# Performance work log

Hardware: AMD Instinct MI355X
Metric: run time of the kernel (lower is better)

The kernel has to match this reference:

```python
import jax, jax.numpy as jnp
import numpy as np

NUM_NODES = 100000
FEAT_DIM = 256
H1 = 256
H2 = 256
NUM_CLASSES = 64
B = 4096
F1 = 25
F2 = 10


def setup_inputs() -> dict:
    key = jax.random.key(0)
    k0, k1, k2, ke, kw1, kw2, kw3 = jax.random.split(key, 7)
    T0 = jax.random.randint(k0, (B,), 0, NUM_NODES)
    T1 = jax.random.randint(k1, (B, F1), 0, NUM_NODES)
    T2 = jax.random.randint(k2, (B * F1, F2), 0, NUM_NODES)
    emb = jax.random.normal(ke, (NUM_NODES, FEAT_DIM), dtype=jnp.float32)
    # nn.Linear(in, out, bias=False) stores weight as [out, in]
    W1 = jax.random.normal(kw1, (H1, 2 * FEAT_DIM), dtype=jnp.float32) * (1.0 / np.sqrt(2 * FEAT_DIM))
    W2 = jax.random.normal(kw2, (H2, 2 * H1), dtype=jnp.float32) * (1.0 / np.sqrt(2 * H1))
    W3 = jax.random.normal(kw3, (NUM_CLASSES, H2), dtype=jnp.float32) * (1.0 / np.sqrt(H2))
    return {"T0": T0, "T1": T1, "T2": T2, "emb": emb, "W1": W1, "W2": W2, "W3": W3}


def reference(T0, T1, T2, emb, W1, W2, W3):
    # hop-0 roots: [B, D]; hop-1 neighbor mean: [B, D]
    feat_0 = emb[T0]
    x = emb[T1].mean(axis=1)
    h0 = jax.nn.relu(jnp.concatenate([feat_0, x], axis=1) @ W1.T)  # [B, H1]
    # dropout is identity in eval mode (p applied only in training)
    # hop-1 nodes with hop-2 neighbor mean: [B*F1, D] each
    feat_1 = emb[T1].reshape(-1, FEAT_DIM)
    x2 = emb[T2].mean(axis=1)  # [B*F1, D]
    h1 = jax.nn.relu(jnp.concatenate([feat_1, x2], axis=1) @ W1.T)  # [B*F1, H1]
    h1 = h1.reshape(B, F1, H1).mean(axis=1)  # [B, H1]
    combined = jnp.concatenate([h0, h1], axis=1)  # [B, 2*H1]
    embedding = jax.nn.relu(combined @ W2.T)  # [B, H2]
    scores = embedding @ W3.T  # [B, C]
    return scores
```

## Files before the change

kernel.cpp:

```cpp
#include <hip/hip_runtime.h>
#include <hip/hip_bf16.h>


typedef __bf16  bf16x8 __attribute__((ext_vector_type(8)));
typedef __bf16  bf16x4 __attribute__((ext_vector_type(4)));
typedef float   f32x4  __attribute__((ext_vector_type(4)));
typedef float   f32x2  __attribute__((ext_vector_type(2)));

#define BATCH     4096
#define F1        25
#define F2        10
#define NNODES    100000
#define ZY_NT     3125
#define ZY_BLOCKS 512

__device__ __forceinline__ uint2 pack4_bf16(float a, float b, float c, float d) {
    union { __bf16 h[4]; uint2 u; } p;
    p.h[0] = (__bf16)a; p.h[1] = (__bf16)b; p.h[2] = (__bf16)c; p.h[3] = (__bf16)d;
    return p.u;
}

__global__ __launch_bounds__(256) void cvt_bf16_8(const float* __restrict__ in,
                                                  __bf16* __restrict__ out, int n8) {
    int i = blockIdx.x * 256 + threadIdx.x;
    if (i < n8) {
        float4 v0 = reinterpret_cast<const float4*>(in)[i * 2];
        float4 v1 = reinterpret_cast<const float4*>(in)[i * 2 + 1];
        uint4 o;
        uint2 a = pack4_bf16(v0.x, v0.y, v0.z, v0.w);
        uint2 b = pack4_bf16(v1.x, v1.y, v1.z, v1.w);
        o.x = a.x; o.y = a.y; o.z = b.x; o.w = b.y;
        reinterpret_cast<uint4*>(out)[i] = o;
    }
}

__global__ __launch_bounds__(256) void prep_wzy(const float* __restrict__ W1,
                                                __bf16* __restrict__ Wzy) {
    int i = blockIdx.x * 256 + threadIdx.x;
    int r  = i >> 5;
    int c0 = (i & 31) * 8;
    const float* src = (r < 256) ? (W1 + (size_t)r * 512 + c0)
                                 : (W1 + (size_t)(r - 256) * 512 + 256 + c0);
    float4 a = reinterpret_cast<const float4*>(src)[0];
    float4 b = reinterpret_cast<const float4*>(src)[1];
    uint4 o;
    uint2 pa = pack4_bf16(a.x, a.y, a.z, a.w);
    uint2 pb = pack4_bf16(b.x, b.y, b.z, b.w);
    o.x = pa.x; o.y = pa.y; o.z = pb.x; o.w = pb.y;
    *reinterpret_cast<uint4*>(Wzy + (size_t)r * 256 + c0) = o;
}

__global__ __launch_bounds__(512, 2) void gemm_ZY(const float* __restrict__ emb,
                                                  const __bf16* __restrict__ Wzy,
                                                  __bf16* __restrict__ Ztab,
                                                  unsigned char* __restrict__ Y8) {
    __shared__ __align__(16) char Abuf[2][16384];
    __shared__ __align__(16) __bf16 Ybuf[8][32][72];
    const int tid  = threadIdx.x;
    const int wid  = tid >> 6;
    const int lane = tid & 63;
    const int lr   = lane & 15;
    const int kg   = lane >> 4;
    const int n0   = wid * 64;

    bf16x8 wfrag[4][8];
    {
        const __bf16* Wb = Wzy + (size_t)(n0 + lr) * 256 + kg * 8;
#pragma unroll
        for (int ni = 0; ni < 4; ++ni)
#pragma unroll
            for (int kt = 0; kt < 8; ++kt)
                wfrag[ni][kt] = *reinterpret_cast<const bf16x8*>(Wb + ni * 16 * 256 + kt * 32);
    }

    const int o0   = tid * 32;
    const int rs   = o0 >> 9;
    const int x0   = o0 & 511;
    const int sw0  = rs * 512 + ((x0)      ^ ((rs & 7) << 4));
    const int sw1  = rs * 512 + ((x0 + 16) ^ ((rs & 7) << 4));

    int t = blockIdx.x;
    float4 ld0[4];
    {
        const float4* src = reinterpret_cast<const float4*>(emb + (size_t)t * 8192 + tid * 16);
#pragma unroll
        for (int q = 0; q < 4; ++q) ld0[q] = src[q];
    }
    int cur = 0;

    for (; t < ZY_NT; t += ZY_BLOCKS) {
        {
            bf16x8 c0v, c1v;
#pragma unroll
            for (int e = 0; e < 4; ++e) {
                c0v[e]     = (__bf16)ld0[0][e];
                c0v[4 + e] = (__bf16)ld0[1][e];
                c1v[e]     = (__bf16)ld0[2][e];
                c1v[4 + e] = (__bf16)ld0[3][e];
            }
            *reinterpret_cast<bf16x8*>(Abuf[cur] + sw0) = c0v;
            *reinterpret_cast<bf16x8*>(Abuf[cur] + sw1) = c1v;
        }
        int tn = t + ZY_BLOCKS;
        float4 ld1[4] = {};
        if (tn < ZY_NT) {
            const float4* src = reinterpret_cast<const float4*>(emb + (size_t)tn * 8192 + tid * 16);
#pragma unroll
            for (int q = 0; q < 4; ++q) ld1[q] = src[q];
        }
        __syncthreads();

        f32x4 acc[2][4] = {};
        const char* Ab = Abuf[cur];
#pragma unroll
        for (int kt = 0; kt < 8; ++kt) {
            bf16x8 a[2];
#pragma unroll
            for (int mi = 0; mi < 2; ++mi) {
                int r  = mi * 16 + lr;
                int by = kt * 64 + kg * 16;
                a[mi] = *reinterpret_cast<const bf16x8*>(Ab + r * 512 + (by ^ ((r & 7) << 4)));
            }
#pragma unroll
            for (int mi = 0; mi < 2; ++mi)
#pragma unroll
                for (int ni = 0; ni < 4; ++ni)
                    acc[mi][ni] = __builtin_amdgcn_mfma_f32_16x16x32_bf16(a[mi], wfrag[ni][kt], acc[mi][ni], 0, 0, 0);
        }

        const int orow = (lane >> 4) * 4;
        const int ocol = lane & 15;
        const int m0   = t * 32;
#pragma unroll
        for (int mi = 0; mi < 2; ++mi)
#pragma unroll
            for (int ni = 0; ni < 4; ++ni)
#pragma unroll
                for (int j = 0; j < 4; ++j)
                    Ybuf[wid][mi * 16 + orow + j][ni * 16 + ocol] = (__bf16)acc[mi][ni][j];
        const int row = lane & 31;
        const int cg  = (lane >> 5) * 32;
        if (wid < 4) {
#pragma unroll
            for (int q = 0; q < 4; ++q) {
                bf16x8 v = *reinterpret_cast<bf16x8*>(&Ybuf[wid][row][cg + q * 8]);
                *reinterpret_cast<bf16x8*>(Ztab + (size_t)(m0 + row) * 256 + n0 + cg + q * 8) = v;
            }
        } else {
#pragma unroll
            for (int q = 0; q < 4; ++q) {
                bf16x8 v = *reinterpret_cast<bf16x8*>(&Ybuf[wid][row][cg + q * 8]);
                int w0 = 0, w1 = 0;
                w0 = __builtin_amdgcn_cvt_pk_fp8_f32((float)v[0], (float)v[1], w0, false);
                w0 = __builtin_amdgcn_cvt_pk_fp8_f32((float)v[2], (float)v[3], w0, true);
                w1 = __builtin_amdgcn_cvt_pk_fp8_f32((float)v[4], (float)v[5], w1, false);
                w1 = __builtin_amdgcn_cvt_pk_fp8_f32((float)v[6], (float)v[7], w1, true);
                uint2 o; o.x = (unsigned)w0; o.y = (unsigned)w1;
                *reinterpret_cast<uint2*>(Y8 + (size_t)(m0 + row) * 256 + (n0 - 256) + cg + q * 8) = o;
            }
        }

#pragma unroll
        for (int q = 0; q < 4; ++q) ld0[q] = ld1[q];
        cur ^= 1;
    }
}

__global__ __launch_bounds__(256) void agg_kernel(const int* __restrict__ T0,
                                                  const int* __restrict__ T1,
                                                  const int* __restrict__ T2,
                                                  const __bf16* __restrict__ Ztab,
                                                  const unsigned char* __restrict__ Y8,
                                                  __bf16* __restrict__ comb) {
    __shared__ float red1[4][256];
    __shared__ float red0[4][256];
    const int b    = blockIdx.x;
    const int wv   = threadIdx.x >> 6;
    const int lane = threadIdx.x & 63;
    float macc[4] = {};
    float h0y[4]  = {};

    for (int f = wv; f < F1; f += 4) {
        const int r  = __builtin_amdgcn_readfirstlane(b * F1 + f);
        const int t1 = T1[r];
        int idx[F2];
#pragma unroll
        for (int j = 0; j < F2; ++j) idx[j] = T2[(size_t)r * F2 + j];

        bf16x4 z = *reinterpret_cast<const bf16x4*>(Ztab + (size_t)t1 * 256 + lane * 4);
        unsigned int y1 = *reinterpret_cast<const unsigned int*>(Y8 + (size_t)t1 * 256 + lane * 4);
        float sy[4] = {};
#pragma unroll
        for (int j = 0; j < F2; ++j) {
            unsigned int yv = *reinterpret_cast<const unsigned int*>(Y8 + (size_t)idx[j] * 256 + lane * 4);
            f32x2 lo = __builtin_amdgcn_cvt_pk_f32_fp8(yv, false);
            f32x2 hi = __builtin_amdgcn_cvt_pk_f32_fp8(yv, true);
            sy[0] += lo[0]; sy[1] += lo[1]; sy[2] += hi[0]; sy[3] += hi[1];
        }
        {
            f32x2 lo = __builtin_amdgcn_cvt_pk_f32_fp8(y1, false);
            f32x2 hi = __builtin_amdgcn_cvt_pk_f32_fp8(y1, true);
            h0y[0] += lo[0]; h0y[1] += lo[1]; h0y[2] += hi[0]; h0y[3] += hi[1];
        }
#pragma unroll
        for (int e = 0; e < 4; ++e)
            macc[e] += fmaxf((float)z[e] + sy[e] * (1.0f / F2), 0.0f);
    }

    float4 t1v; t1v.x = macc[0]; t1v.y = macc[1]; t1v.z = macc[2]; t1v.w = macc[3];
    float4 t0v; t0v.x = h0y[0];  t0v.y = h0y[1];  t0v.z = h0y[2];  t0v.w = h0y[3];
    *reinterpret_cast<float4*>(&red1[wv][lane * 4]) = t1v;
    *reinterpret_cast<float4*>(&red0[wv][lane * 4]) = t0v;
    __syncthreads();

    const int col = threadIdx.x;
    float s1 = red1[0][col] + red1[1][col] + red1[2][col] + red1[3][col];
    float s0 = red0[0][col] + red0[1][col] + red0[2][col] + red0[3][col];
    const int t0 = T0[b];
    float z0 = (float)Ztab[(size_t)t0 * 256 + col];
    comb[(size_t)b * 512 + col]       = (__bf16)fmaxf(z0 + s0 * (1.0f / F1), 0.0f);
    comb[(size_t)b * 512 + 256 + col] = (__bf16)(s1 * (1.0f / F1));
}

__global__ __launch_bounds__(256) void gemm_relu_bf16(const __bf16* __restrict__ A,
                                                      const __bf16* __restrict__ W,
                                                      __bf16* __restrict__ C,
                                                      int K, int ldc) {
    int wid  = threadIdx.x >> 6;
    int lane = threadIdx.x & 63;
    int m0 = blockIdx.x * 128 + (wid >> 1) * 64;
    int n0 = blockIdx.y * 128 + (wid & 1) * 64;
    int lr = lane & 15;
    int kg = lane >> 4;

    f32x4 acc[4][4] = {};
    const __bf16* Abase = A + (size_t)(m0 + lr) * K + kg * 8;
    const __bf16* Wbase = W + (size_t)(n0 + lr) * K + kg * 8;

    for (int kt = 0; kt < K; kt += 32) {
        bf16x8 a[4], b[4];
#pragma unroll
        for (int i = 0; i < 4; ++i)
            a[i] = *reinterpret_cast<const bf16x8*>(Abase + (size_t)i * 16 * K + kt);
#pragma unroll
        for (int i = 0; i < 4; ++i)
            b[i] = *reinterpret_cast<const bf16x8*>(Wbase + (size_t)i * 16 * K + kt);
#pragma unroll
        for (int mi = 0; mi < 4; ++mi)
#pragma unroll
            for (int ni = 0; ni < 4; ++ni)
                acc[mi][ni] = __builtin_amdgcn_mfma_f32_16x16x32_bf16(a[mi], b[ni], acc[mi][ni], 0, 0, 0);
    }

    int orow = (lane >> 4) * 4;
    int ocol = lane & 15;
#pragma unroll
    for (int mi = 0; mi < 4; ++mi)
#pragma unroll
        for (int ni = 0; ni < 4; ++ni)
#pragma unroll
            for (int j = 0; j < 4; ++j) {
                float v = fmaxf(acc[mi][ni][j], 0.0f);
                C[(size_t)(m0 + mi * 16 + orow + j) * ldc + (n0 + ni * 16 + ocol)] = (__bf16)v;
            }
}

__global__ __launch_bounds__(256) void gemm_out(const __bf16* __restrict__ A,
                                                const __bf16* __restrict__ W,
                                                float* __restrict__ C) {
    const int K = 256;
    int wid  = threadIdx.x >> 6;
    int lane = threadIdx.x & 63;
    int m0 = blockIdx.x * 128 + wid * 32;
    int lr = lane & 15;
    int kg = lane >> 4;

    f32x4 acc[2][4] = {};
    const __bf16* Abase = A + (size_t)(m0 + lr) * K + kg * 8;
    const __bf16* Wbase = W + (size_t)lr * K + kg * 8;

    for (int kt = 0; kt < K; kt += 32) {
        bf16x8 a[2], b[4];
#pragma unroll
        for (int i = 0; i < 2; ++i)
            a[i] = *reinterpret_cast<const bf16x8*>(Abase + (size_t)i * 16 * K + kt);
#pragma unroll
        for (int i = 0; i < 4; ++i)
            b[i] = *reinterpret_cast<const bf16x8*>(Wbase + (size_t)i * 16 * K + kt);
#pragma unroll
        for (int mi = 0; mi < 2; ++mi)
#pragma unroll
            for (int ni = 0; ni < 4; ++ni)
                acc[mi][ni] = __builtin_amdgcn_mfma_f32_16x16x32_bf16(a[mi], b[ni], acc[mi][ni], 0, 0, 0);
    }

    int orow = (lane >> 4) * 4;
    int ocol = lane & 15;
#pragma unroll
    for (int mi = 0; mi < 2; ++mi)
#pragma unroll
        for (int ni = 0; ni < 4; ++ni)
#pragma unroll
            for (int j = 0; j < 4; ++j)
                C[(size_t)(m0 + mi * 16 + orow + j) * 64 + (ni * 16 + ocol)] = acc[mi][ni][j];
}

extern "C" void kernel_launch(void* const* d_in, const int* in_sizes, int n_in,
                              void* d_out, int out_size, void* d_ws, size_t ws_size,
                              hipStream_t stream) {
    const int*   T0  = (const int*)d_in[0];
    const int*   T1  = (const int*)d_in[1];
    const int*   T2  = (const int*)d_in[2];
    const float* emb = (const float*)d_in[3];
    const float* W1  = (const float*)d_in[4];
    const float* W2  = (const float*)d_in[5];
    const float* W3  = (const float*)d_in[6];
    float* out = (float*)d_out;

    char* ws = (char*)d_ws;
    __bf16*        Wzy  = (__bf16*)(ws);
    __bf16*        W2b  = (__bf16*)(ws + 262144);
    __bf16*        W3b  = (__bf16*)(ws + 524288);
    __bf16*        comb = (__bf16*)(ws + 557056);
    __bf16*        embd = (__bf16*)(ws + 4751360);
    __bf16*        Ztab = (__bf16*)(ws + 6848512);
    unsigned char* Y8   = (unsigned char*)(ws + 58048512);

    prep_wzy<<<dim3(64), dim3(256), 0, stream>>>(W1, Wzy);
    cvt_bf16_8<<<dim3(64), dim3(256), 0, stream>>>(W2, W2b, 131072 / 8);
    cvt_bf16_8<<<dim3(8), dim3(256), 0, stream>>>(W3, W3b, 16384 / 8);

    gemm_ZY<<<dim3(ZY_BLOCKS), dim3(512), 0, stream>>>(emb, Wzy, Ztab, Y8);

    agg_kernel<<<dim3(BATCH), dim3(256), 0, stream>>>(T0, T1, T2, Ztab, Y8, comb);

    gemm_relu_bf16<<<dim3(BATCH / 128, 2), dim3(256), 0, stream>>>(comb, W2b, embd, 512, 256);
    gemm_out<<<dim3(BATCH / 128), dim3(256), 0, stream>>>(embd, W3b, out);
}
```

Baseline: 134.7 us.

## Merge weight prep kernels and deepen gemm_ZY prefetch to two tiles

The three weight-conversion launches are merged into one prep_weights kernel, saving two launches. In gemm_ZY the embedding tile loads are now coalesced across threads (stride 512 float4 per q) and prefetched two tiles ahead, with register buffers indexed by stage parity. The launch bounds hint rises from 2 to 4 waves per SIMD, which could force register spills given the large wfrag array. The goal is to hide more HBM latency on the streaming read of emb.

```diff
diff --git a/kernel.cpp b/kernel.cpp
--- a/kernel.cpp
+++ b/kernel.cpp
@@ -20,10 +20,31 @@
     return p.u;
 }
 
-__global__ __launch_bounds__(256) void cvt_bf16_8(const float* __restrict__ in,
-                                                  __bf16* __restrict__ out, int n8) {
-    int i = blockIdx.x * 256 + threadIdx.x;
-    if (i < n8) {
+__global__ __launch_bounds__(256) void prep_weights(const float* __restrict__ W1,
+                                                    const float* __restrict__ W2,
+                                                    const float* __restrict__ W3,
+                                                    __bf16* __restrict__ Wzy,
+                                                    __bf16* __restrict__ W2b,
+                                                    __bf16* __restrict__ W3b) {
+    int blk = blockIdx.x;
+    if (blk < 64) {
+        int i = blk * 256 + threadIdx.x;
+        int r  = i >> 5;
+        int c0 = (i & 31) * 8;
+        const float* src = (r < 256) ? (W1 + (size_t)r * 512 + c0)
+                                     : (W1 + (size_t)(r - 256) * 512 + 256 + c0);
+        float4 a = reinterpret_cast<const float4*>(src)[0];
+        float4 b = reinterpret_cast<const float4*>(src)[1];
+        uint4 o;
+        uint2 pa = pack4_bf16(a.x, a.y, a.z, a.w);
+        uint2 pb = pack4_bf16(b.x, b.y, b.z, b.w);
+        o.x = pa.x; o.y = pa.y; o.z = pb.x; o.w = pb.y;
+        *reinterpret_cast<uint4*>(Wzy + (size_t)r * 256 + c0) = o;
+    } else {
+        const float* in; __bf16* out;
+        int i;
+        if (blk < 128) { in = W2; out = W2b; i = (blk - 64) * 256 + threadIdx.x; }
+        else           { in = W3; out = W3b; i = (blk - 128) * 256 + threadIdx.x; }
         float4 v0 = reinterpret_cast<const float4*>(in)[i * 2];
         float4 v1 = reinterpret_cast<const float4*>(in)[i * 2 + 1];
         uint4 o;
@@ -34,23 +55,7 @@
     }
 }
 
-__global__ __launch_bounds__(256) void prep_wzy(const float* __restrict__ W1,
-                                                __bf16* __restrict__ Wzy) {
-    int i = blockIdx.x * 256 + threadIdx.x;
-    int r  = i >> 5;
-    int c0 = (i & 31) * 8;
-    const float* src = (r < 256) ? (W1 + (size_t)r * 512 + c0)
-                                 : (W1 + (size_t)(r - 256) * 512 + 256 + c0);
-    float4 a = reinterpret_cast<const float4*>(src)[0];
-    float4 b = reinterpret_cast<const float4*>(src)[1];
-    uint4 o;
-    uint2 pa = pack4_bf16(a.x, a.y, a.z, a.w);
-    uint2 pb = pack4_bf16(b.x, b.y, b.z, b.w);
-    o.x = pa.x; o.y = pa.y; o.z = pb.x; o.w = pb.y;
-    *reinterpret_cast<uint4*>(Wzy + (size_t)r * 256 + c0) = o;
-}
-
-__global__ __launch_bounds__(512, 2) void gemm_ZY(const float* __restrict__ emb,
+__global__ __launch_bounds__(512, 4) void gemm_ZY(const float* __restrict__ emb,
                                                   const __bf16* __restrict__ Wzy,
                                                   __bf16* __restrict__ Ztab,
                                                   unsigned char* __restrict__ Y8) {
@@ -73,45 +78,47 @@
                 wfrag[ni][kt] = *reinterpret_cast<const bf16x8*>(Wb + ni * 16 * 256 + kt * 32);
     }
 
-    const int o0   = tid * 32;
-    const int rs   = o0 >> 9;
-    const int x0   = o0 & 511;
-    const int sw0  = rs * 512 + ((x0)      ^ ((rs & 7) << 4));
-    const int sw1  = rs * 512 + ((x0 + 16) ^ ((rs & 7) << 4));
-
+    int soff[4];
+#pragma unroll
+    for (int q = 0; q < 4; ++q) {
+        int e  = q * 2048 + tid * 4;
+        int r  = e >> 8;
+        int cb = (e & 255) * 2;
+        soff[q] = r * 512 + (cb ^ ((r & 7) << 4));
+    }
+
+    float4 ld[2][4];
     int t = blockIdx.x;
-    float4 ld0[4];
-    {
-        const float4* src = reinterpret_cast<const float4*>(emb + (size_t)t * 8192 + tid * 16);
-#pragma unroll
-        for (int q = 0; q < 4; ++q) ld0[q] = src[q];
-    }
-    int cur = 0;
-
-    for (; t < ZY_NT; t += ZY_BLOCKS) {
+    if (t < ZY_NT) {
+        const float4* src = reinterpret_cast<const float4*>(emb + (size_t)t * 8192);
+#pragma unroll
+        for (int q = 0; q < 4; ++q) ld[0][q] = src[q * 512 + tid];
+    }
+    if (t + ZY_BLOCKS < ZY_NT) {
+        const float4* src = reinterpret_cast<const float4*>(emb + (size_t)(t + ZY_BLOCKS) * 8192);
+#pragma unroll
+        for (int q = 0; q < 4; ++q) ld[1][q] = src[q * 512 + tid];
+    }
+
+    int p = 0;
+    for (; t < ZY_NT; t += ZY_BLOCKS, p ^= 1) {
+#pragma unroll
+        for (int q = 0; q < 4; ++q) {
+            float4 v = ld[p][q];
+            *reinterpret_cast<uint2*>(Abuf[p] + soff[q]) = pack4_bf16(v.x, v.y, v.z, v.w);
+        }
         {
-            bf16x8 c0v, c1v;
-#pragma unroll
-            for (int e = 0; e < 4; ++e) {
-                c0v[e]     = (__bf16)ld0[0][e];
-                c0v[4 + e] = (__bf16)ld0[1][e];
-                c1v[e]     = (__bf16)ld0[2][e];
-                c1v[4 + e] = (__bf16)ld0[3][e];
-            }
-            *reinterpret_cast<bf16x8*>(Abuf[cur] + sw0) = c0v;
-            *reinterpret_cast<bf16x8*>(Abuf[cur] + sw1) = c1v;
-        }
-        int tn = t + ZY_BLOCKS;
-        float4 ld1[4] = {};
-        if (tn < ZY_NT) {
-            const float4* src = reinterpret_cast<const float4*>(emb + (size_t)tn * 8192 + tid * 16);
-#pragma unroll
-            for (int q = 0; q < 4; ++q) ld1[q] = src[q];
+            int tn = t + 2 * ZY_BLOCKS;
+            if (tn < ZY_NT) {
+                const float4* src = reinterpret_cast<const float4*>(emb + (size_t)tn * 8192);
+#pragma unroll
+                for (int q = 0; q < 4; ++q) ld[p][q] = src[q * 512 + tid];
+            }
         }
         __syncthreads();
 
         f32x4 acc[2][4] = {};
-        const char* Ab = Abuf[cur];
+        const char* Ab = Abuf[p];
 #pragma unroll
         for (int kt = 0; kt < 8; ++kt) {
             bf16x8 a[2];
@@ -159,10 +166,6 @@
                 *reinterpret_cast<uint2*>(Y8 + (size_t)(m0 + row) * 256 + (n0 - 256) + cg + q * 8) = o;
             }
         }
-
-#pragma unroll
-        for (int q = 0; q < 4; ++q) ld0[q] = ld1[q];
-        cur ^= 1;
     }
 }
 
@@ -326,9 +329,7 @@
     __bf16*        Ztab = (__bf16*)(ws + 6848512);
     unsigned char* Y8   = (unsigned char*)(ws + 58048512);
 
-    prep_wzy<<<dim3(64), dim3(256), 0, stream>>>(W1, Wzy);
-    cvt_bf16_8<<<dim3(64), dim3(256), 0, stream>>>(W2, W2b, 131072 / 8);
-    cvt_bf16_8<<<dim3(8), dim3(256), 0, stream>>>(W3, W3b, 16384 / 8);
+    prep_weights<<<dim3(136), dim3(256), 0, stream>>>(W1, W2, W3, Wzy, W2b, W3b);
 
     gemm_ZY<<<dim3(ZY_BLOCKS), dim3(512), 0, stream>>>(emb, Wzy, Ztab, Y8);
 
```

After: 228.5 us. 1.7x slower.
